# Kernel optimization log

Measured on AMD Instinct MI355X. Metric: run time of the kernel, lower is better.

Reference implementation:

```python
import jax, jax.numpy as jnp
import numpy as np

D_MODEL = 2048
N_HEADS = 16
N_KV_HEADS = 4
HEAD_DIM = D_MODEL // N_HEADS  # 128
WINDOW = 512
SOFTCAP = 50.0
ROPE_THETA = 10000.0
BATCH = 2
SEQ = 2048
NEG_INF = -1e30


def _rope_cos_sin(seq_len, head_dim, theta):
    # inv_freq over half the head dim, duplicated (HF rotate_half convention)
    inv_freq = 1.0 / (theta ** (jnp.arange(0, head_dim, 2, dtype=jnp.float32) / head_dim))
    freqs = jnp.arange(seq_len, dtype=jnp.float32)[:, None] * inv_freq[None, :]  # [S, hd/2]
    emb = jnp.concatenate([freqs, freqs], axis=-1)  # [S, hd]
    return jnp.cos(emb), jnp.sin(emb)


def _rotate_half(x):
    x1, x2 = jnp.split(x, 2, axis=-1)
    return jnp.concatenate([-x2, x1], axis=-1)


def _apply_rope(x, cos, sin):
    # x: [B, S, H, hd]; cos/sin: [S, hd] broadcast over batch & heads (unsqueeze_dim=2)
    c = cos[None, :, None, :]
    s = sin[None, :, None, :]
    return x * c + _rotate_half(x) * s


def setup_inputs() -> dict:
    key = jax.random.key(0)
    ks = jax.random.split(key, 5)
    scale_p = 1.0 / np.sqrt(D_MODEL)
    return {
        "hidden_states": jax.random.normal(ks[0], (BATCH, SEQ, D_MODEL), dtype=jnp.float32),
        "wq": jax.random.normal(ks[1], (N_HEADS * HEAD_DIM, D_MODEL), dtype=jnp.float32) * scale_p,
        "wk": jax.random.normal(ks[2], (N_KV_HEADS * HEAD_DIM, D_MODEL), dtype=jnp.float32) * scale_p,
        "wv": jax.random.normal(ks[3], (N_KV_HEADS * HEAD_DIM, D_MODEL), dtype=jnp.float32) * scale_p,
        "wo": jax.random.normal(ks[4], (D_MODEL, N_HEADS * HEAD_DIM), dtype=jnp.float32) * scale_p,
    }


def reference(hidden_states, wq, wk, wv, wo):
    B, S, _ = hidden_states.shape
    groups = N_HEADS // N_KV_HEADS
    scale = HEAD_DIM ** -0.5

    q = (hidden_states @ wq.T).reshape(B, S, N_HEADS, HEAD_DIM)
    k = (hidden_states @ wk.T).reshape(B, S, N_KV_HEADS, HEAD_DIM)
    v = (hidden_states @ wv.T).reshape(B, S, N_KV_HEADS, HEAD_DIM)

    cos, sin = _rope_cos_sin(S, HEAD_DIM, ROPE_THETA)
    q = _apply_rope(q, cos, sin)
    k = _apply_rope(k, cos, sin)

    # GQA head expansion: each kv head serves `groups` query heads
    k = jnp.repeat(k, groups, axis=2)  # [B, S, H, hd]
    v = jnp.repeat(v, groups, axis=2)

    scores = jnp.einsum("bqhd,bkhd->bhqk", q, k) * scale
    scores = SOFTCAP * jnp.tanh(scores / SOFTCAP)

    i = jnp.arange(S)[:, None]
    j = jnp.arange(S)[None, :]
    allowed = (j <= i) & (j > i - WINDOW)  # causal + sliding window
    scores = jnp.where(allowed[None, None], scores, NEG_INF)

    attn = jax.nn.softmax(scores, axis=-1)
    out = jnp.einsum("bhqk,bkhd->bqhd", attn, v).reshape(B, S, N_HEADS * HEAD_DIM)
    return out @ wo.T
```

## Files before the change

### kernel.cpp

```cpp
#include <hip/hip_runtime.h>
#include <hip/hip_bf16.h>
#include <stdint.h>

#define DM    2048
#define NH    16
#define NKVH  4
#define HD    128
#define WIN   512
#define SEQL  2048
#define BAT   2
#define MR    (BAT*SEQL)
#define NQKV  3072
#define QKSCALE 0.08838834764831845f
#define CAP   50.0f
#define C1F (QKSCALE * 2.0f * 1.4426950408889634f / CAP)
#define C2F (-144.26950408889634f)

typedef unsigned short u16;
typedef __attribute__((ext_vector_type(8))) short short8;
typedef __attribute__((ext_vector_type(4))) float f32x4;
typedef __attribute__((ext_vector_type(16))) float f32x16;

__device__ __forceinline__ u16 f2bf(float f) {
  union { float f; uint32_t u; } v; v.f = f;
  uint32_t r = v.u + 0x7FFFu + ((v.u >> 16) & 1u);
  return (u16)(r >> 16);
}
__device__ __forceinline__ float bf2f(u16 h) {
  union { uint32_t u; float f; } v; v.u = ((uint32_t)h) << 16; return v.f;
}
__device__ __forceinline__ void gld16(const void* g, void* l) {
  __builtin_amdgcn_global_load_lds((const __attribute__((address_space(1))) void*)g,
                                   (__attribute__((address_space(3))) void*)l,
                                   16, 0, 0);
}
__device__ __forceinline__ float exp_softcap(float sv) {
  float t = __builtin_amdgcn_exp2f(sv);
  float u = __builtin_amdgcn_rcpf(t + 1.0f);
  return __builtin_amdgcn_exp2f(u * C2F);
}

__global__ void k_prep(const float* __restrict__ hs, const float* __restrict__ wq,
                       const float* __restrict__ wk, const float* __restrict__ wv,
                       const float* __restrict__ wo,
                       u16* __restrict__ A_bf, u16* __restrict__ Wqkv,
                       u16* __restrict__ Wo,
                       float* __restrict__ cosT, float* __restrict__ sinT) {
  const int bid = blockIdx.x;
  if (bid < 18432) {
    const int g = bid * 256 + threadIdx.x;
    const float* src; u16* dst; int off;
    if (g < 2097152)      { src = hs; dst = A_bf;           off = 0; }
    else if (g < 3145728) { src = wq; dst = Wqkv;           off = 2097152; }
    else if (g < 3407872) { src = wk; dst = Wqkv + 4194304; off = 3145728; }
    else if (g < 3670016) { src = wv; dst = Wqkv + 5242880; off = 3407872; }
    else                  { src = wo; dst = Wo;             off = 3670016; }
    const int li = g - off;
    float4 v = ((const float4*)src)[li];
    ushort4 o;
    o.x = f2bf(v.x); o.y = f2bf(v.y); o.z = f2bf(v.z); o.w = f2bf(v.w);
    ((ushort4*)dst)[li] = o;
  } else {
    const int rt = (bid - 18432) * 256 + threadIdx.x;
    const int s = rt >> 6, i = rt & 63;
    float invf = expf(-(float)i * (9.210340371976184f / 64.0f));
    float a = (float)s * invf;
    cosT[rt] = cosf(a);
    sinT[rt] = sinf(a);
  }
}

__global__ __launch_bounds__(256, 3) void k_gemm_qkv(const u16* __restrict__ A,
                                                     const u16* __restrict__ Bm,
                                                     u16* __restrict__ qrout,
                                                     u16* __restrict__ krout,
                                                     u16* __restrict__ vtout,
                                                     const float* __restrict__ cosT,
                                                     const float* __restrict__ sinT) {
  __shared__ __align__(16) u16 ldsA[128 * 64];
  __shared__ __align__(16) u16 ldsB[128 * 64];
  const int t = threadIdx.x;
  const int K = DM;

  const int nwg  = gridDim.x * gridDim.y;
  const int flat = blockIdx.y * gridDim.x + blockIdx.x;
  const int cpx  = nwg >> 3;
  const int swz  = (flat & 7) * cpx + (flat >> 3);
  const int bn = swz % gridDim.x, bm = swz / gridDim.x;

  const int m0 = bm * 128, n0 = bn * 128;
  const int lane = t & 63, wid = t >> 6;
  const int lr = lane & 15, lk = lane >> 4;
  const int wr = wid * 32;
  const int nt = K >> 6;
  (void)n0;

  const int srow = t >> 3;
  const int scol = (((t & 7) ^ (srow & 7)) << 3);

  f32x4 acc[2][8];
  #pragma unroll
  for (int mi = 0; mi < 2; ++mi)
    #pragma unroll
    for (int ni = 0; ni < 8; ++ni) acc[mi][ni] = f32x4{0.f, 0.f, 0.f, 0.f};

  for (int kt = 0; kt < nt; ++kt) {
    {
      const u16* a0 = A  + (size_t)(m0 + srow) * K + kt * 64 + scol;
      const u16* b0 = Bm + (size_t)(bn * 128 + srow) * K + kt * 64 + scol;
      #pragma unroll
      for (int i = 0; i < 4; ++i) {
        gld16(a0 + (size_t)(i * 32) * K, &ldsA[i * 2048 + t * 8]);
        gld16(b0 + (size_t)(i * 32) * K, &ldsB[i * 2048 + t * 8]);
      }
    }
    __syncthreads();
    #pragma unroll
    for (int ks = 0; ks < 2; ++ks) {
      const int c = ks * 4 + lk;
      short8 af[2], bfv[8];
      #pragma unroll
      for (int mi = 0; mi < 2; ++mi) {
        const int ra = wr + mi * 16 + lr;
        af[mi] = *(const short8*)(ldsA + ra * 64 + ((c ^ (ra & 7)) << 3));
      }
      #pragma unroll
      for (int ni = 0; ni < 8; ++ni) {
        const int rb = ni * 16 + lr;
        bfv[ni] = *(const short8*)(ldsB + rb * 64 + ((c ^ (rb & 7)) << 3));
      }
      #pragma unroll
      for (int mi = 0; mi < 2; ++mi)
        #pragma unroll
        for (int ni = 0; ni < 8; ++ni)
          acc[mi][ni] = __builtin_amdgcn_mfma_f32_16x16x32_bf16(af[mi], bfv[ni], acc[mi][ni], 0, 0, 0);
    }
    if (kt + 1 < nt) __syncthreads();
  }

  const int bb2 = m0 >> 11;

  if (bn < 20) {
    const bool isq = (bn < 16);
    u16* obase = isq ? (qrout + (size_t)(bb2 * NH + bn) * SEQL * HD)
                     : (krout + (size_t)(bb2 * NKVH + (bn - 16)) * SEQL * HD);
    #pragma unroll
    for (int mi = 0; mi < 2; ++mi) {
      const int rbase = m0 + wr + mi * 16 + lk * 4;
      #pragma unroll
      for (int ni = 0; ni < 4; ++ni) {
        const int d64 = ni * 16 + lr;
        #pragma unroll
        for (int r = 0; r < 4; ++r) {
          const int s = (rbase + r) & (SEQL - 1);
          float x = acc[mi][ni][r];
          float y = acc[mi][ni + 4][r];
          float cc = cosT[(s << 6) + d64], ss = sinT[(s << 6) + d64];
          float o0 = x * cc - y * ss;
          float o1 = y * cc + x * ss;
          if (isq) { o0 *= C1F; o1 *= C1F; }
          obase[(size_t)s * HD + d64]      = f2bf(o0);
          obase[(size_t)s * HD + d64 + 64] = f2bf(o1);
        }
      }
    }
  } else {
    const int kvh = bn - 20;
    u16* vb = vtout + (size_t)(bb2 * NKVH + kvh) * HD * SEQL;
    #pragma unroll
    for (int mi = 0; mi < 2; ++mi) {
      const int s0 = (m0 + wr + mi * 16 + lk * 4) & (SEQL - 1);
      #pragma unroll
      for (int ni = 0; ni < 8; ++ni) {
        const int d = ni * 16 + lr;
        ushort4 w4;
        w4.x = f2bf(acc[mi][ni][0]); w4.y = f2bf(acc[mi][ni][1]);
        w4.z = f2bf(acc[mi][ni][2]); w4.w = f2bf(acc[mi][ni][3]);
        *(ushort4*)(vb + (size_t)d * SEQL + s0) = w4;
      }
    }
  }
}

__global__ __launch_bounds__(256, 4) void k_gemm_ao(const u16* __restrict__ A,
                                                    const u16* __restrict__ Bm,
                                                    float* __restrict__ C,
                                                    int N, int K) {
  __shared__ __align__(16) u16 ldsA[128 * 64];
  __shared__ __align__(16) u16 ldsB[64 * 64];
  const int t = threadIdx.x;

  const int nwg  = gridDim.x * gridDim.y;
  const int flat = blockIdx.y * gridDim.x + blockIdx.x;
  const int cpx  = nwg >> 3;
  const int swz  = (flat & 7) * cpx + (flat >> 3);
  const int bn = swz % gridDim.x, bm = swz / gridDim.x;

  const int m0 = bm * 128, n0 = bn * 64;
  const int lane = t & 63, wid = t >> 6;
  const int lr = lane & 15, lk = lane >> 4;
  const int wr = (wid >> 1) * 64, wc = (wid & 1) * 32;
  const int nt = K >> 6;

  const int srow = t >> 3;
  const int scol = (((t & 7) ^ (srow & 7)) << 3);

  f32x4 acc[4][2];
  #pragma unroll
  for (int mi = 0; mi < 4; ++mi)
    #pragma unroll
    for (int ni = 0; ni < 2; ++ni) acc[mi][ni] = f32x4{0.f, 0.f, 0.f, 0.f};

  for (int kt = 0; kt < nt; ++kt) {
    {
      const u16* a0 = A  + (size_t)(m0 + srow) * K + kt * 64 + scol;
      const u16* b0 = Bm + (size_t)(n0 + srow) * K + kt * 64 + scol;
      #pragma unroll
      for (int i = 0; i < 4; ++i)
        gld16(a0 + (size_t)(i * 32) * K, &ldsA[i * 2048 + t * 8]);
      #pragma unroll
      for (int i = 0; i < 2; ++i)
        gld16(b0 + (size_t)(i * 32) * K, &ldsB[i * 2048 + t * 8]);
    }
    __syncthreads();
    #pragma unroll
    for (int ks = 0; ks < 2; ++ks) {
      const int c = ks * 4 + lk;
      short8 af[4], bfv[2];
      #pragma unroll
      for (int mi = 0; mi < 4; ++mi) {
        const int ra = wr + mi * 16 + lr;
        af[mi] = *(const short8*)(ldsA + ra * 64 + ((c ^ (ra & 7)) << 3));
      }
      #pragma unroll
      for (int ni = 0; ni < 2; ++ni) {
        const int rb = wc + ni * 16 + lr;
        bfv[ni] = *(const short8*)(ldsB + rb * 64 + ((c ^ (rb & 7)) << 3));
      }
      #pragma unroll
      for (int mi = 0; mi < 4; ++mi)
        #pragma unroll
        for (int ni = 0; ni < 2; ++ni)
          acc[mi][ni] = __builtin_amdgcn_mfma_f32_16x16x32_bf16(af[mi], bfv[ni], acc[mi][ni], 0, 0, 0);
    }
    if (kt + 1 < nt) __syncthreads();
  }

  #pragma unroll
  for (int mi = 0; mi < 4; ++mi) {
    #pragma unroll
    for (int ni = 0; ni < 2; ++ni) {
      const int r0 = m0 + wr + mi * 16 + lk * 4;
      const int c  = n0 + wc + ni * 16 + lr;
      #pragma unroll
      for (int r = 0; r < 4; ++r)
        C[(size_t)(r0 + r) * N + c] = acc[mi][ni][r];
    }
  }
}

__global__ __launch_bounds__(256, 2) void k_attn(const u16* __restrict__ qr,
                                                 const u16* __restrict__ kr,
                                                 const u16* __restrict__ vt,
                                                 u16* __restrict__ ao) {
  __shared__ __align__(16) u16 kbuf[2][32 * 128];
  __shared__ __align__(16) u16 vbuf[2][128 * 32];

  const int t = threadIdx.x;
  const int wid = t >> 6, lane = t & 63;
  const int l31 = lane & 31, lh = lane >> 5;
  const int h = blockIdx.x, bq = blockIdx.y, b = blockIdx.z;
  const int kvh = h >> 2;
  const int Q0 = bq * 128;
  const int q0w = Q0 + wid * 32;
  const u16* qb = qr + (size_t)(b * NH + h) * SEQL * HD;
  const u16* kb = kr + (size_t)(b * NKVH + kvh) * SEQL * HD;
  const u16* vb = vt + (size_t)(b * NKVH + kvh) * HD * SEQL;

  short8 qf[8];
  #pragma unroll
  for (int ks = 0; ks < 8; ++ks)
    qf[ks] = *(const short8*)(qb + (size_t)(q0w + l31) * HD + ks * 16 + lh * 8);

  f32x16 o[4];
  #pragma unroll
  for (int dt = 0; dt < 4; ++dt)
    #pragma unroll
    for (int i = 0; i < 16; ++i) o[dt][i] = 0.f;
  float lsum = 0.f;

  int lo = Q0 - (WIN - 1); if (lo < 0) lo = 0;
  const int ktlo = lo >> 5, kthi = (Q0 + 127) >> 5;

  auto stageK = [&](int bufi, int kv0) {
    #pragma unroll
    for (int i = 0; i < 2; ++i) {
      int c = t + i * 256;
      int bb = c << 4;
      int sb = bb ^ (((bb >> 8) & 7) << 4);
      gld16(kb + (size_t)(kv0 + (sb >> 8)) * HD + ((sb & 255) >> 1),
            &kbuf[bufi][c << 3]);
    }
  };
  auto stageV = [&](int bufi, int kv0) {
    #pragma unroll
    for (int i = 0; i < 2; ++i) {
      int c = t + i * 256;
      int bb = c << 4;
      int sb = bb ^ (((bb >> 7) & 3) << 4);
      gld16(vb + (size_t)(sb >> 6) * SEQL + kv0 + ((sb & 63) >> 1),
            &vbuf[bufi][c << 3]);
    }
  };

  stageK(0, ktlo << 5);
  stageV(0, ktlo << 5);
  __syncthreads();

  for (int kt = ktlo; kt <= kthi; ++kt) {
    const int cur = kt & 1;
    if (kt < kthi) { stageK(cur ^ 1, (kt + 1) << 5); stageV(cur ^ 1, (kt + 1) << 5); }
    const int kv0 = kt << 5;
    if (kv0 + 31 >= q0w - (WIN - 1) && kv0 <= q0w + 31) {
      f32x16 sv;
      #pragma unroll
      for (int i = 0; i < 16; ++i) sv[i] = 0.f;
      const u16* lks = kbuf[cur];
      #pragma unroll
      for (int ks = 0; ks < 8; ++ks) {
        int bo = (l31 * 256 + ks * 32 + lh * 16) ^ ((l31 & 7) << 4);
        short8 kf = *(const short8*)(lks + (bo >> 1));
        sv = __builtin_amdgcn_mfma_f32_32x32x16_bf16(kf, qf[ks], sv, 0, 0, 0);
      }
      float p[16];
      const bool interior = (kv0 + 31 <= q0w) && (kv0 >= q0w + 32 - WIN);
      if (interior) {
        #pragma unroll
        for (int r = 0; r < 16; ++r) p[r] = exp_softcap(sv[r]);
      } else {
        const int qg = q0w + l31;
        #pragma unroll
        for (int r = 0; r < 16; ++r) {
          const int kg = kv0 + (r & 3) + 8 * (r >> 2) + 4 * lh;
          float e = exp_softcap(sv[r]);
          p[r] = (kg <= qg && kg > qg - WIN) ? e : 0.f;
        }
      }
      #pragma unroll
      for (int r = 0; r < 16; ++r) lsum += p[r];

      uint32_t w[8];
      #pragma unroll
      for (int r2 = 0; r2 < 8; ++r2) {
        __hip_bfloat162 u = __float22bfloat162_rn(float2{p[2 * r2], p[2 * r2 + 1]});
        w[r2] = *(uint32_t*)&u;
      }
      uint32_t z0 = lh ? w[0] : w[2], z1 = lh ? w[1] : w[3];
      uint32_t z2 = lh ? w[4] : w[6], z3 = lh ? w[5] : w[7];
      uint32_t x0 = __shfl_xor((int)z0, 32), x1 = __shfl_xor((int)z1, 32);
      uint32_t x2 = __shfl_xor((int)z2, 32), x3 = __shfl_xor((int)z3, 32);
      union U8 { uint32_t u[4]; short8 s; };
      U8 pa0, pa1;
      pa0.u[0] = lh ? x0 : w[0];  pa0.u[1] = lh ? x1 : w[1];
      pa0.u[2] = lh ? w[2] : x0;  pa0.u[3] = lh ? w[3] : x1;
      pa1.u[0] = lh ? x2 : w[4];  pa1.u[1] = lh ? x3 : w[5];
      pa1.u[2] = lh ? w[6] : x2;  pa1.u[3] = lh ? w[7] : x3;

      const u16* lvs = vbuf[cur];
      #pragma unroll
      for (int ks2 = 0; ks2 < 2; ++ks2) {
        const short8 paf = ks2 ? pa1.s : pa0.s;
        #pragma unroll
        for (int dt = 0; dt < 4; ++dt) {
          int row = dt * 32 + l31;
          int bo = (row * 64 + ks2 * 32 + lh * 16) ^ (((row >> 1) & 3) << 4);
          short8 vf = *(const short8*)(lvs + (bo >> 1));
          o[dt] = __builtin_amdgcn_mfma_f32_32x32x16_bf16(paf, vf, o[dt], 0, 0, 0);
        }
      }
    }
    __syncthreads();
  }

  lsum += __shfl_xor(lsum, 32);
  float linv = 1.0f / lsum;
  #pragma unroll
  for (int rr = 0; rr < 4; ++rr) {
    #pragma unroll
    for (int r = 0; r < 4; ++r) {
      const int crow = r + 8 * rr + 4 * lh;
      float inv = __shfl(linv, crow);
      const int srow = q0w + crow;
      u16* op = ao + (size_t)(b * SEQL + srow) * DM + h * HD;
      #pragma unroll
      for (int dt = 0; dt < 4; ++dt)
        op[dt * 32 + l31] = f2bf(o[dt][rr * 4 + r] * inv);
    }
  }
}

extern "C" void kernel_launch(void* const* d_in, const int* in_sizes, int n_in,
                              void* d_out, int out_size, void* d_ws, size_t ws_size,
                              hipStream_t stream) {
  (void)in_sizes; (void)n_in; (void)out_size; (void)ws_size;
  const float* hs = (const float*)d_in[0];
  const float* wq = (const float*)d_in[1];
  const float* wk = (const float*)d_in[2];
  const float* wv = (const float*)d_in[3];
  const float* wo = (const float*)d_in[4];
  float* out = (float*)d_out;

  u16* ws    = (u16*)d_ws;
  u16* A_bf  = ws;
  u16* Wqkv  = A_bf + 8388608;
  u16* Wo    = Wqkv + 6291456;
  u16* q_r   = Wo + 4194304;
  u16* k_r   = q_r + 8388608;
  u16* vTb   = k_r + 2097152;
  float* cosT = (float*)(vTb + 2097152);
  float* sinT = cosT + 131072;
  u16* aout = A_bf;

  k_prep<<<18944, 256, 0, stream>>>(hs, wq, wk, wv, wo, A_bf, Wqkv, Wo, cosT, sinT);

  k_gemm_qkv<<<dim3(NQKV / 128, MR / 128), 256, 0, stream>>>(A_bf, Wqkv, q_r, k_r, vTb,
                                                             cosT, sinT);

  k_attn<<<dim3(NH, SEQL / 128, BAT), 256, 0, stream>>>(q_r, k_r, vTb, aout);

  k_gemm_ao<<<dim3(DM / 64, MR / 128), 256, 0, stream>>>(aout, Wo, out, DM, DM);
}
```

Before: 164.0 us.

## Double-buffer LDS in QKV GEMM with interleaved prefetch and MFMA phases

Result: slower. 234.2 us (+42.8%).

```diff
diff --git a/kernel.cpp b/kernel.cpp
--- a/kernel.cpp
+++ b/kernel.cpp
@@ -70,15 +70,15 @@
   }
 }
 
-__global__ __launch_bounds__(256, 3) void k_gemm_qkv(const u16* __restrict__ A,
+__global__ __launch_bounds__(256, 2) void k_gemm_qkv(const u16* __restrict__ A,
                                                      const u16* __restrict__ Bm,
                                                      u16* __restrict__ qrout,
                                                      u16* __restrict__ krout,
                                                      u16* __restrict__ vtout,
                                                      const float* __restrict__ cosT,
                                                      const float* __restrict__ sinT) {
-  __shared__ __align__(16) u16 ldsA[128 * 64];
-  __shared__ __align__(16) u16 ldsB[128 * 64];
+  __shared__ __align__(16) u16 ldsA[2][128 * 64];
+  __shared__ __align__(16) u16 ldsB[2][128 * 64];
   const int t = threadIdx.x;
   const int K = DM;
 
@@ -93,10 +93,14 @@
   const int lr = lane & 15, lk = lane >> 4;
   const int wr = wid * 32;
   const int nt = K >> 6;
-  (void)n0;
 
   const int srow = t >> 3;
   const int scol = (((t & 7) ^ (srow & 7)) << 3);
+  const u16* aBase = A  + (size_t)(m0 + srow) * K + scol;
+  const u16* bBase = Bm + (size_t)(n0 + srow) * K + scol;
+
+  #define STA(p, x, i) gld16(aBase + (size_t)((i) * 32) * K + (x) * 64, &ldsA[p][(i) * 2048 + t * 8])
+  #define STB(p, x, i) gld16(bBase + (size_t)((i) * 32) * K + (x) * 64, &ldsB[p][(i) * 2048 + t * 8])
 
   f32x4 acc[2][8];
   #pragma unroll
@@ -104,39 +108,84 @@
     #pragma unroll
     for (int ni = 0; ni < 8; ++ni) acc[mi][ni] = f32x4{0.f, 0.f, 0.f, 0.f};
 
+  STA(0, 0, 0); STA(0, 0, 1); STA(0, 0, 2); STA(0, 0, 3);
+  STB(0, 0, 0); STB(0, 0, 1); STB(0, 0, 2); STB(0, 0, 3);
+  STA(1, 1, 0); STA(1, 1, 1); STA(1, 1, 2); STA(1, 1, 3);
+  STB(1, 1, 0); STB(1, 1, 1); STB(1, 1, 2);
+
   for (int kt = 0; kt < nt; ++kt) {
-    {
-      const u16* a0 = A  + (size_t)(m0 + srow) * K + kt * 64 + scol;
-      const u16* b0 = Bm + (size_t)(bn * 128 + srow) * K + kt * 64 + scol;
-      #pragma unroll
-      for (int i = 0; i < 4; ++i) {
-        gld16(a0 + (size_t)(i * 32) * K, &ldsA[i * 2048 + t * 8]);
-        gld16(b0 + (size_t)(i * 32) * K, &ldsB[i * 2048 + t * 8]);
-      }
-    }
-    __syncthreads();
-    #pragma unroll
-    for (int ks = 0; ks < 2; ++ks) {
-      const int c = ks * 4 + lk;
-      short8 af[2], bfv[8];
-      #pragma unroll
-      for (int mi = 0; mi < 2; ++mi) {
-        const int ra = wr + mi * 16 + lr;
-        af[mi] = *(const short8*)(ldsA + ra * 64 + ((c ^ (ra & 7)) << 3));
-      }
-      #pragma unroll
-      for (int ni = 0; ni < 8; ++ni) {
-        const int rb = ni * 16 + lr;
-        bfv[ni] = *(const short8*)(ldsB + rb * 64 + ((c ^ (rb & 7)) << 3));
-      }
+    const int cur = kt & 1;
+    const u16* la = ldsA[cur];
+    const u16* lb = ldsB[cur];
+
+    if (kt + 1 < nt) {
+      STB(cur ^ 1, kt + 1, 3);
+      asm volatile("s_waitcnt vmcnt(8)" ::: "memory");
+    } else {
+      asm volatile("s_waitcnt vmcnt(0)" ::: "memory");
+    }
+    __builtin_amdgcn_s_barrier();
+    __builtin_amdgcn_sched_barrier(0);
+    short8 af[2][2], bfv[2][2];
+    #pragma unroll
+    for (int mi = 0; mi < 2; ++mi) {
+      const int ra = wr + mi * 16 + lr;
+      #pragma unroll
+      for (int ks = 0; ks < 2; ++ks)
+        af[mi][ks] = *(const short8*)(la + ra * 64 + (((ks * 4 + lk) ^ (ra & 7)) << 3));
+    }
+    #pragma unroll
+    for (int ni = 0; ni < 2; ++ni) {
+      const int rb = ni * 16 + lr;
+      #pragma unroll
+      for (int ks = 0; ks < 2; ++ks)
+        bfv[ni][ks] = *(const short8*)(lb + rb * 64 + (((ks * 4 + lk) ^ (rb & 7)) << 3));
+    }
+    asm volatile("s_waitcnt lgkmcnt(0)" ::: "memory");
+    __builtin_amdgcn_sched_barrier(0);
+    __builtin_amdgcn_s_setprio(1);
+    #pragma unroll
+    for (int mi = 0; mi < 2; ++mi)
+      #pragma unroll
+      for (int ni = 0; ni < 2; ++ni)
+        #pragma unroll
+        for (int ks = 0; ks < 2; ++ks)
+          acc[mi][ni] = __builtin_amdgcn_mfma_f32_16x16x32_bf16(af[mi][ks], bfv[ni][ks], acc[mi][ni], 0, 0, 0);
+    __builtin_amdgcn_s_setprio(0);
+    __builtin_amdgcn_s_barrier();
+
+    #pragma unroll
+    for (int n2 = 1; n2 < 4; ++n2) {
+      if (kt + 2 < nt) {
+        if (n2 == 1) { STA(cur, kt + 2, 0); STA(cur, kt + 2, 1);
+                       STA(cur, kt + 2, 2); STA(cur, kt + 2, 3);
+                       STB(cur, kt + 2, 0); }
+        else if (n2 == 2) { STB(cur, kt + 2, 1); }
+        else              { STB(cur, kt + 2, 2); }
+      }
+      #pragma unroll
+      for (int ni = 0; ni < 2; ++ni) {
+        const int rb = (n2 * 2 + ni) * 16 + lr;
+        #pragma unroll
+        for (int ks = 0; ks < 2; ++ks)
+          bfv[ni][ks] = *(const short8*)(lb + rb * 64 + (((ks * 4 + lk) ^ (rb & 7)) << 3));
+      }
+      asm volatile("s_waitcnt lgkmcnt(0)" ::: "memory");
+      __builtin_amdgcn_sched_barrier(0);
+      __builtin_amdgcn_s_setprio(1);
       #pragma unroll
       for (int mi = 0; mi < 2; ++mi)
         #pragma unroll
-        for (int ni = 0; ni < 8; ++ni)
-          acc[mi][ni] = __builtin_amdgcn_mfma_f32_16x16x32_bf16(af[mi], bfv[ni], acc[mi][ni], 0, 0, 0);
-    }
-    if (kt + 1 < nt) __syncthreads();
-  }
+        for (int ni = 0; ni < 2; ++ni)
+          #pragma unroll
+          for (int ks = 0; ks < 2; ++ks)
+            acc[mi][n2 * 2 + ni] = __builtin_amdgcn_mfma_f32_16x16x32_bf16(af[mi][ks], bfv[ni][ks], acc[mi][n2 * 2 + ni], 0, 0, 0);
+      __builtin_amdgcn_s_setprio(0);
+      __builtin_amdgcn_s_barrier();
+    }
+  }
+  #undef STA
+  #undef STB
 
   const int bb2 = m0 >> 11;
 
```
